# Optimization experiments

Measured on AMD Instinct MI355X. Metric: run time of the kernel, lower is better.

Reference implementation:

```python
import jax, jax.numpy as jnp
import numpy as np

# Hyperparameters matching init_kwargs
LR = 0.02
AT = 0.3
DSBETA = 0.1
EPS_DS = 0.5

B, D, N = 8192, 1024, 4096


def setup_inputs() -> dict:
    key = jax.random.key(0)
    k0, k1, k2, k3 = jax.random.split(key, 4)
    x = jax.random.normal(k0, (B, D), dtype=jnp.float32)
    weights = jax.random.normal(k1, (N, D), dtype=jnp.float32)
    relevance = jax.random.uniform(k2, (N, D), dtype=jnp.float32)
    moving_avg = jax.random.uniform(k3, (N, D), dtype=jnp.float32)
    node_control = jnp.ones((N,), dtype=jnp.float32)
    return {"x": x, "weights": weights, "relevance": relevance,
            "moving_avg": moving_avg, "node_control": node_control}


def reference(x, weights, relevance, moving_avg, node_control):
    n, d = weights.shape
    # pairwise squared distances [B, N] via one GEMM
    x2 = jnp.sum(x * x, axis=1, keepdims=True)            # [B,1]
    w2 = jnp.sum(weights * weights, axis=1)[None, :]      # [1,N]
    dists = x2 + w2 - 2.0 * jnp.matmul(x, weights.T)      # [B,N]
    # weighted_distance + activation
    rsum = jnp.sum(relevance, axis=1)                     # [N]
    dw = dists * (rsum / d)[None, :]
    dw = jnp.where(jnp.isnan(dw), 0.0, dw)
    act = (rsum[None, :] / (rsum[None, :] + dw + 1e-7)) * node_control[None, :]
    act_max = jnp.max(act, axis=1)                        # [B]
    idx = jnp.argmax(act, axis=1)                         # [B] winner per sample
    # high-activation mask; group samples by winner node (unique_node_diff_vectorized
    # == per-node mean of assigned high samples, done with segment_sum at fixed N)
    high = (act_max >= AT).astype(x.dtype)                # [B]
    counts = jax.ops.segment_sum(high, idx, num_segments=n)               # [N]
    sums = jax.ops.segment_sum(x * high[:, None], idx, num_segments=n)    # [N,D]
    has = (counts > 0).astype(x.dtype)[:, None]           # [N,1] nodes with >=1 high sample
    mean_s = sums / jnp.maximum(counts, 1.0)[:, None]     # [N,D] updatable_samples (dense)
    # update_node math (EMA moving_avg -> relevance -> weight update)
    a = LR * DSBETA
    distance = jnp.abs(mean_s - weights)
    mavg_new = a * distance + (1.0 - a) * moving_avg
    mx = jnp.max(mavg_new, axis=1, keepdims=True)
    mn = jnp.min(mavg_new, axis=1, keepdims=True)
    avg = jnp.mean(mavg_new, axis=1, keepdims=True)
    rel_new = 1.0 / (1.0 + jnp.exp((mavg_new - avg) / (EPS_DS * (mx - mn))))
    rel_new = jnp.where(jnp.isnan(rel_new), 1.0, rel_new)
    w_new = weights + LR * (mean_s - weights)
    # Original returns rows only for unique winning nodes (dynamic shape); here we
    # return fixed-shape [N,D] arrays masked to zero for nodes with no high sample.
    return (mean_s * has, w_new * has, rel_new * has)
```

## Files before the change

### kernel.cpp

```cpp
#include <hip/hip_runtime.h>
#include <stdint.h>


#define B_DIM 8192
#define D_DIM 1024
#define N_DIM 4096
#define ND ((size_t)N_DIM * D_DIM)
#define LRc 0.02f
#define ATc 0.3f
#define EMAc (0.02f * 0.1f)
#define QS 32.0f
#define INV_QS2 (1.0f / (QS * QS))
#define MARGIN_G 10.0f

typedef int intv4 __attribute__((ext_vector_type(4)));

__device__ __forceinline__ void async16(void* lds, const void* g) {
    __builtin_amdgcn_global_load_lds((const __attribute__((address_space(1))) void*)g,
                                     (__attribute__((address_space(3))) void*)lds, 16, 0, 0);
}

__device__ __forceinline__ int q8(float v) {
    return (int)rintf(fminf(fmaxf(v * QS, -127.0f), 127.0f));
}

__device__ __forceinline__ unsigned pack4(float4 v) {
    return (unsigned)(q8(v.x) & 255) | ((unsigned)(q8(v.y) & 255) << 8)
         | ((unsigned)(q8(v.z) & 255) << 16) | ((unsigned)(q8(v.w) & 255) << 24);
}

__global__ __launch_bounds__(256) void prep_k(const float* __restrict__ x, const float* __restrict__ w,
                                              const float* __restrict__ rel,
                                              signed char* __restrict__ xq, signed char* __restrict__ wq,
                                              float* __restrict__ x2p, float* __restrict__ w2p,
                                              float* __restrict__ rsump, float* __restrict__ gbp) {
    const int lane = threadIdx.x & 63, wave = threadIdx.x >> 6;
    const int row = (blockIdx.x << 2) + wave;
    if (row < B_DIM) {
        const float4* xr = (const float4*)(x + (size_t)row * D_DIM);
        unsigned* xqr = (unsigned*)(xq + (size_t)row * D_DIM);
        float ss = 0.f;
#pragma unroll
        for (int j = 0; j < 4; ++j) {
            const float4 v = xr[lane + j * 64];
            ss += v.x * v.x + v.y * v.y + v.z * v.z + v.w * v.w;
            xqr[lane + j * 64] = pack4(v);
        }
#pragma unroll
        for (int o = 32; o; o >>= 1) ss += __shfl_xor(ss, o);
        if (lane == 0) x2p[row] = ss;
    } else {
        const int n = row - B_DIM;
        const float4* wr = (const float4*)(w + (size_t)n * D_DIM);
        const float4* rr = (const float4*)(rel + (size_t)n * D_DIM);
        unsigned* wqr = (unsigned*)(wq + (size_t)n * D_DIM);
        float ss = 0.f, rs = 0.f;
#pragma unroll
        for (int j = 0; j < 4; ++j) {
            const float4 v = wr[lane + j * 64];
            const float4 rv = rr[lane + j * 64];
            ss += v.x * v.x + v.y * v.y + v.z * v.z + v.w * v.w;
            rs += rv.x + rv.y + rv.z + rv.w;
            wqr[lane + j * 64] = pack4(v);
        }
#pragma unroll
        for (int o = 32; o; o >>= 1) { ss += __shfl_xor(ss, o); rs += __shfl_xor(rs, o); }
        if (lane == 0) {
            w2p[n] = ss;
            rsump[n] = rs;
            gbp[n] = ss + (1e-7f * (float)D_DIM) / rs;
        }
    }
}

__global__ __launch_bounds__(512, 2) void gemm_k(const signed char* __restrict__ xq,
                                                 const signed char* __restrict__ wq,
                                                 const float* __restrict__ gbp,
                                                 unsigned short* __restrict__ resq,
                                                 float* __restrict__ tminp) {
    extern __shared__ char smem[];
    const int t = threadIdx.x;
    const int mt = blockIdx.x & 31;
    const int nt = blockIdx.x >> 5;
    const int m0 = mt * 256, n0 = nt * 256;
    const int lane = t & 63, wave = t >> 6;
    const int q = lane >> 4, ln = lane & 15;
    const int wm = wave >> 2, wn = wave & 3;

    intv4 acc[8][4];
#pragma unroll
    for (int i = 0; i < 8; ++i)
#pragma unroll
        for (int j = 0; j < 4; ++j) acc[i][j] = (intv4){0, 0, 0, 0};

    int gOff[4], lOff[4];
#pragma unroll
    for (int s = 0; s < 4; ++s) {
        const int L = t + s * 512;
        const int r = L >> 3;
        gOff[s] = r * D_DIM + ((L & 7) ^ (r & 7)) * 16;
        lOff[s] = L * 16;
    }
    const signed char* Ap = xq + (size_t)m0 * D_DIM;
    const signed char* Bp = wq + (size_t)n0 * D_DIM;

    const int baseA = (wm * 128 + ln) * 128;
    const int baseB = (wn * 64 + ln) * 128;

#define STAGE_KT(kt, slot) do {                                                     \
        char* sa_ = smem + (slot) * 65536;                                          \
        const int k0_ = (kt) * 128;                                                 \
        _Pragma("unroll")                                                           \
        for (int s_ = 0; s_ < 4; ++s_) async16(sa_ + lOff[s_], Ap + gOff[s_] + k0_);\
        _Pragma("unroll")                                                           \
        for (int s_ = 0; s_ < 4; ++s_) async16(sa_ + 32768 + lOff[s_], Bp + gOff[s_] + k0_); \
    } while (0)

#define COMPUTE_KT(slot) do {                                                       \
        const char* sa_ = smem + (slot) * 65536;                                    \
        const char* sb_ = sa_ + 32768;                                              \
        _Pragma("unroll")                                                           \
        for (int ks = 0; ks < 2; ++ks) {                                            \
            const int jx = ((ks * 4 + q) ^ (ln & 7)) * 16;                          \
            intv4 a[8], b[4];                                                       \
            _Pragma("unroll")                                                       \
            for (int i = 0; i < 8; ++i) a[i] = *(const intv4*)(sa_ + baseA + i * 2048 + jx); \
            _Pragma("unroll")                                                       \
            for (int j = 0; j < 4; ++j) b[j] = *(const intv4*)(sb_ + baseB + j * 2048 + jx); \
            __builtin_amdgcn_s_setprio(1);                                          \
            _Pragma("unroll")                                                       \
            for (int i = 0; i < 8; ++i)                                             \
                _Pragma("unroll")                                                   \
                for (int j = 0; j < 4; ++j)                                         \
                    acc[i][j] = __builtin_amdgcn_mfma_i32_16x16x64_i8(a[i], b[j], acc[i][j], 0, 0, 0); \
            __builtin_amdgcn_s_setprio(0);                                          \
        }                                                                           \
    } while (0)

    STAGE_KT(0, 0);
#pragma unroll
    for (int kt = 0; kt < 8; ++kt) {
        if (kt < 7) {
            STAGE_KT(kt + 1, (kt + 1) & 1);
            asm volatile("s_waitcnt vmcnt(8)" ::: "memory");
        } else {
            asm volatile("s_waitcnt vmcnt(0)" ::: "memory");
        }
        __builtin_amdgcn_s_barrier();
        COMPUTE_KT(kt & 1);
        asm volatile("" ::: "memory");
        __builtin_amdgcn_s_barrier();
    }
#undef STAGE_KT
#undef COMPUTE_KT

    float gbv[4];
#pragma unroll
    for (int j = 0; j < 4; ++j) gbv[j] = gbp[n0 + wn * 64 + j * 16 + ln];
    const float cf = 2.0f * INV_QS2;
    const int tile64 = nt * 4 + wn;
#pragma unroll
    for (int i = 0; i < 8; ++i) {
#pragma unroll
        for (int r = 0; r < 4; ++r) {
            const int m = m0 + wm * 128 + i * 16 + q * 4 + r;
            float g[4];
            float mn = 3.4e38f;
#pragma unroll
            for (int j = 0; j < 4; ++j) {
                g[j] = gbv[j] - cf * (float)acc[i][j][r];
                mn = fminf(mn, g[j]);
            }
#pragma unroll
            for (int o = 1; o < 16; o <<= 1) mn = fminf(mn, __shfl_xor(mn, o));
            if (ln == 0) tminp[(size_t)m * 64 + tile64] = mn;
            unsigned u = 0;
#pragma unroll
            for (int j = 0; j < 4; ++j) {
                int a4 = (int)rintf(g[j] - mn);
                a4 = (a4 > 15) ? 15 : a4;
                u |= (unsigned)a4 << (4 * j);
            }
            resq[(size_t)m * 1024 + tile64 * 16 + ln] = (unsigned short)u;
        }
    }
}

__global__ __launch_bounds__(256) void resolve_k(const unsigned short* __restrict__ resq,
                                                 const float* __restrict__ tminp,
                                                 const float* __restrict__ x2p,
                                                 const float* __restrict__ x, const float* __restrict__ w,
                                                 const float* __restrict__ w2p, const float* __restrict__ rsump,
                                                 const float* __restrict__ ncp,
                                                 int* __restrict__ win) {
    const int lane = threadIdx.x & 63, wave = threadIdx.x >> 6;
    const int b = (blockIdx.x << 2) + wave;
    const float tv = tminp[(size_t)b * 64 + lane];
    float rowmin = tv;
#pragma unroll
    for (int o = 32; o; o >>= 1) rowmin = fminf(rowmin, __shfl_xor(rowmin, o));
    const float th = rowmin + MARGIN_G;
    const float thq = th + 0.5f;
    const unsigned long long tmask = __ballot(tv <= th);
    const float x2v = x2p[b];
    const unsigned short* rrow = resq + (size_t)b * 1024;
    const int nibsh = (lane >> 4) * 4;

    int cnt = 0, myn = -1;
    float myg = 0.0f;
    unsigned long long tm = tmask;
    while (tm) {
        const int tt = __ffsll((long long)tm) - 1;
        tm &= tm - 1;
        const float tb = __shfl(tv, tt);
        const unsigned short pv = rrow[tt * 16 + (lane & 15)];
        const float g = tb + (float)((pv >> nibsh) & 15);
        const bool c = (g <= thq);
        cnt += __popcll(__ballot(c));
        if (c && myn < 0) { myn = tt * 64 + lane; myg = g; }
    }

    if (cnt == 1) {
        if (myn >= 0) {
            const float act = ncp[myn] * (float)D_DIM / ((float)D_DIM + x2v + myg);
            win[b] = (act >= ATc) ? myn : -1;
        }
    } else {
        const float4* xr = (const float4*)(x + (size_t)b * D_DIM);
        float4 xv[4];
#pragma unroll
        for (int j = 0; j < 4; ++j) xv[j] = xr[lane + j * 64];
        float best_act = -1.0f;
        int best_n = N_DIM;
        tm = tmask;
        while (tm) {
            const int tt = __ffsll((long long)tm) - 1;
            tm &= tm - 1;
            const float tb = __shfl(tv, tt);
            const unsigned short pv = rrow[tt * 16 + (lane & 15)];
            const float g = tb + (float)((pv >> nibsh) & 15);
            unsigned long long cm = __ballot(g <= thq);
            while (cm) {
                const int l = __ffsll((long long)cm) - 1;
                cm &= cm - 1;
                const int n = tt * 64 + l;
                const float4* wr = (const float4*)(w + (size_t)n * D_DIM);
                float p = 0.f;
#pragma unroll
                for (int j = 0; j < 4; ++j) {
                    const float4 wv = wr[lane + j * 64];
                    p += xv[j].x * wv.x + xv[j].y * wv.y + xv[j].z * wv.z + xv[j].w * wv.w;
                }
#pragma unroll
                for (int o = 32; o; o >>= 1) p += __shfl_xor(p, o);
                const float dist = x2v + w2p[n] - 2.0f * p;
                const float rs = rsump[n];
                const float dw = dist * rs * (1.0f / (float)D_DIM);
                const float a = rs * ncp[n] / (rs + dw + 1e-7f);
                if (a > best_act || (a == best_act && n < best_n)) { best_act = a; best_n = n; }
            }
        }
        if (lane == 0) win[b] = (best_act >= ATc) ? best_n : -1;
    }
}

__global__ __launch_bounds__(256) void finalize_k(const float* __restrict__ x, const float* __restrict__ w,
                                                  const float* __restrict__ mavg, const int* __restrict__ win,
                                                  float* __restrict__ out) {
    const int n = blockIdx.x, t = threadIdx.x;
    __shared__ unsigned short list[B_DIM];
    __shared__ int cnt;
    __shared__ float smax[4], smin[4], ssum[4];
    if (t == 0) cnt = 0;
    __syncthreads();
    const int4* wp = (const int4*)win;
#pragma unroll
    for (int k = 0; k < 8; ++k) {
        const int4 v = wp[k * 256 + t];
        const int b0 = (k * 256 + t) * 4;
        if (v.x == n) list[atomicAdd(&cnt, 1)] = (unsigned short)(b0 + 0);
        if (v.y == n) list[atomicAdd(&cnt, 1)] = (unsigned short)(b0 + 1);
        if (v.z == n) list[atomicAdd(&cnt, 1)] = (unsigned short)(b0 + 2);
        if (v.w == n) list[atomicAdd(&cnt, 1)] = (unsigned short)(b0 + 3);
    }
    __syncthreads();
    const int c = cnt;
    float4 s = {0.f, 0.f, 0.f, 0.f};
    for (int e = 0; e < c; ++e) {
        const float4 xv = ((const float4*)(x + (size_t)list[e] * D_DIM))[t];
        s.x += xv.x; s.y += xv.y; s.z += xv.z; s.w += xv.w;
    }
    const float has = (c > 0) ? 1.0f : 0.0f;
    const float invc = 1.0f / fmaxf((float)c, 1.0f);
    const size_t base4 = (size_t)n * (D_DIM / 4);
    const float4 wv = ((const float4*)w)[base4 + t];
    const float4 mk = ((const float4*)mavg)[base4 + t];
    float4 ms, mv;
    ms.x = s.x * invc; ms.y = s.y * invc; ms.z = s.z * invc; ms.w = s.w * invc;
    mv.x = EMAc * fabsf(ms.x - wv.x) + (1.0f - EMAc) * mk.x;
    mv.y = EMAc * fabsf(ms.y - wv.y) + (1.0f - EMAc) * mk.y;
    mv.z = EMAc * fabsf(ms.z - wv.z) + (1.0f - EMAc) * mk.z;
    mv.w = EMAc * fabsf(ms.w - wv.w) + (1.0f - EMAc) * mk.w;
    float lmax = fmaxf(fmaxf(mv.x, mv.y), fmaxf(mv.z, mv.w));
    float lmin = fminf(fminf(mv.x, mv.y), fminf(mv.z, mv.w));
    float lsum = mv.x + mv.y + mv.z + mv.w;
#pragma unroll
    for (int o = 32; o; o >>= 1) {
        lmax = fmaxf(lmax, __shfl_xor(lmax, o));
        lmin = fminf(lmin, __shfl_xor(lmin, o));
        lsum += __shfl_xor(lsum, o);
    }
    const int wave = t >> 6, lane = t & 63;
    if (lane == 0) { smax[wave] = lmax; smin[wave] = lmin; ssum[wave] = lsum; }
    __syncthreads();
    const float mx = fmaxf(fmaxf(smax[0], smax[1]), fmaxf(smax[2], smax[3]));
    const float mn = fminf(fminf(smin[0], smin[1]), fminf(smin[2], smin[3]));
    const float avg = (ssum[0] + ssum[1] + ssum[2] + ssum[3]) * (1.0f / (float)D_DIM);
    const float scale = 0.5f * (mx - mn);
    const float invs = (scale > 0.0f) ? 1.0f / scale : 0.0f;
    float4 relv;
    if (scale > 0.0f) {
        relv.x = 1.0f / (1.0f + __expf((mv.x - avg) * invs));
        relv.y = 1.0f / (1.0f + __expf((mv.y - avg) * invs));
        relv.z = 1.0f / (1.0f + __expf((mv.z - avg) * invs));
        relv.w = 1.0f / (1.0f + __expf((mv.w - avg) * invs));
    } else {
        relv.x = relv.y = relv.z = relv.w = 1.0f;
    }
    float4* o0 = (float4*)out;
    float4 r0, r1, r2;
    r0.x = ms.x * has; r0.y = ms.y * has; r0.z = ms.z * has; r0.w = ms.w * has;
    r1.x = (wv.x + LRc * (ms.x - wv.x)) * has;
    r1.y = (wv.y + LRc * (ms.y - wv.y)) * has;
    r1.z = (wv.z + LRc * (ms.z - wv.z)) * has;
    r1.w = (wv.w + LRc * (ms.w - wv.w)) * has;
    r2.x = relv.x * has; r2.y = relv.y * has; r2.z = relv.z * has; r2.w = relv.w * has;
    o0[base4 + t] = r0;
    o0[ND / 4 + base4 + t] = r1;
    o0[2 * (ND / 4) + base4 + t] = r2;
}

extern "C" void kernel_launch(void* const* d_in, const int* in_sizes, int n_in,
                              void* d_out, int out_size, void* d_ws, size_t ws_size,
                              hipStream_t stream) {
    const float* x    = (const float*)d_in[0];
    const float* w    = (const float*)d_in[1];
    const float* rel  = (const float*)d_in[2];
    const float* mavg = (const float*)d_in[3];
    const float* nc   = (const float*)d_in[4];
    float* out = (float*)d_out;

    char* p = (char*)d_ws;
    size_t off = 0;
    auto take = [&](size_t bytes) -> char* {
        char* r = p + off;
        off += (bytes + 255) & ~(size_t)255;
        return r;
    };
    signed char* xq = (signed char*)take((size_t)B_DIM * D_DIM);
    signed char* wq = (signed char*)take((size_t)N_DIM * D_DIM);
    float* x2       = (float*)take((size_t)B_DIM * 4);
    float* w2       = (float*)take((size_t)N_DIM * 4);
    float* rsum     = (float*)take((size_t)N_DIM * 4);
    float* gb       = (float*)take((size_t)N_DIM * 4);
    unsigned short* resq = (unsigned short*)take((size_t)B_DIM * 1024 * 2);
    float* tminp    = (float*)take((size_t)B_DIM * 64 * 4);
    int* win        = (int*)take((size_t)B_DIM * 4);

    static bool attr_set = false;
    if (!attr_set) {
        (void)hipFuncSetAttribute(reinterpret_cast<const void*>(gemm_k),
                                  hipFuncAttributeMaxDynamicSharedMemorySize, 131072);
        attr_set = true;
    }

    prep_k<<<(B_DIM + N_DIM) / 4, 256, 0, stream>>>(x, w, rel, xq, wq, x2, w2, rsum, gb);
    gemm_k<<<512, 512, 131072, stream>>>(xq, wq, gb, resq, tminp);
    resolve_k<<<B_DIM / 4, 256, 0, stream>>>(resq, tminp, x2, x, w, w2, rsum, nc, win);
    finalize_k<<<N_DIM, 256, 0, stream>>>(x, w, mavg, win, out);
}
```

Measured before the change: 207.3 us.

## Split int8 GEMM K-tiles into half-stages with finer-grained async prefetch

```diff
diff --git a/kernel.cpp b/kernel.cpp
--- a/kernel.cpp
+++ b/kernel.cpp
@@ -93,66 +93,67 @@
 #pragma unroll
         for (int j = 0; j < 4; ++j) acc[i][j] = (intv4){0, 0, 0, 0};
 
-    int gOff[4], lOff[4];
-#pragma unroll
-    for (int s = 0; s < 4; ++s) {
-        const int L = t + s * 512;
-        const int r = L >> 3;
-        gOff[s] = r * D_DIM + ((L & 7) ^ (r & 7)) * 16;
-        lOff[s] = L * 16;
-    }
+    const int ls0 = t * 16;
+    const int row0 = t >> 2;
+    const int go0 = row0 * 1024 + (((t & 3) ^ ((row0 >> 1) & 3)) * 16);
+
     const signed char* Ap = xq + (size_t)m0 * D_DIM;
     const signed char* Bp = wq + (size_t)n0 * D_DIM;
 
-    const int baseA = (wm * 128 + ln) * 128;
-    const int baseB = (wn * 64 + ln) * 128;
-
-#define STAGE_KT(kt, slot) do {                                                     \
-        char* sa_ = smem + (slot) * 65536;                                          \
-        const int k0_ = (kt) * 128;                                                 \
-        _Pragma("unroll")                                                           \
-        for (int s_ = 0; s_ < 4; ++s_) async16(sa_ + lOff[s_], Ap + gOff[s_] + k0_);\
-        _Pragma("unroll")                                                           \
-        for (int s_ = 0; s_ < 4; ++s_) async16(sa_ + 32768 + lOff[s_], Bp + gOff[s_] + k0_); \
+    const int aBase = (wm * 128 + ln) * 64;
+    const int bBase = (wn * 64 + ln) * 64 + 32768;
+    const int cslot = (q ^ ((ln >> 1) & 3)) * 16;
+
+#define STG(kt_, kh_, isB_) do {                                                     \
+        char* d_ = smem + ((kt_) & 1) * 65536 + (isB_) * 32768 + (kh_) * 16384;      \
+        const signed char* g_ = ((isB_) ? Bp : Ap) + (kt_) * 128 + (kh_) * 64 + go0; \
+        async16(d_ + ls0, g_);                                                       \
+        async16(d_ + ls0 + 8192, g_ + 131072);                                       \
     } while (0)
 
-#define COMPUTE_KT(slot) do {                                                       \
-        const char* sa_ = smem + (slot) * 65536;                                    \
-        const char* sb_ = sa_ + 32768;                                              \
-        _Pragma("unroll")                                                           \
-        for (int ks = 0; ks < 2; ++ks) {                                            \
-            const int jx = ((ks * 4 + q) ^ (ln & 7)) * 16;                          \
-            intv4 a[8], b[4];                                                       \
-            _Pragma("unroll")                                                       \
-            for (int i = 0; i < 8; ++i) a[i] = *(const intv4*)(sa_ + baseA + i * 2048 + jx); \
-            _Pragma("unroll")                                                       \
-            for (int j = 0; j < 4; ++j) b[j] = *(const intv4*)(sb_ + baseB + j * 2048 + jx); \
-            __builtin_amdgcn_s_setprio(1);                                          \
-            _Pragma("unroll")                                                       \
-            for (int i = 0; i < 8; ++i)                                             \
-                _Pragma("unroll")                                                   \
-                for (int j = 0; j < 4; ++j)                                         \
-                    acc[i][j] = __builtin_amdgcn_mfma_i32_16x16x64_i8(a[i], b[j], acc[i][j], 0, 0, 0); \
-            __builtin_amdgcn_s_setprio(0);                                          \
-        }                                                                           \
+    STG(0, 0, 0); STG(0, 0, 1); STG(0, 1, 0); STG(0, 1, 1); STG(1, 0, 0); STG(1, 0, 1);
+    asm volatile("s_waitcnt vmcnt(8)" ::: "memory");
+    __builtin_amdgcn_s_barrier();
+
+#define VM8 asm volatile("s_waitcnt vmcnt(8)" ::: "memory")
+#define VM4 asm volatile("s_waitcnt vmcnt(4)" ::: "memory")
+#define VM0 asm volatile("s_waitcnt vmcnt(0)" ::: "memory")
+
+#define PH(kt_, ks_, ih_, STMT_STAGE, STMT_WAIT) do {                                \
+        const char* base_ = smem + ((kt_) & 1) * 65536 + (ks_) * 16384;              \
+        intv4 a_[4], b_[4];                                                          \
+        _Pragma("unroll")                                                            \
+        for (int i_ = 0; i_ < 4; ++i_)                                               \
+            a_[i_] = *(const intv4*)(base_ + aBase + (ih_) * 4096 + i_ * 1024 + cslot); \
+        _Pragma("unroll")                                                            \
+        for (int j_ = 0; j_ < 4; ++j_)                                               \
+            b_[j_] = *(const intv4*)(base_ + bBase + j_ * 1024 + cslot);             \
+        STMT_STAGE;                                                                  \
+        STMT_WAIT;                                                                   \
+        __builtin_amdgcn_s_barrier();                                                \
+        __builtin_amdgcn_s_setprio(1);                                               \
+        _Pragma("unroll")                                                            \
+        for (int i_ = 0; i_ < 4; ++i_)                                               \
+            _Pragma("unroll")                                                        \
+            for (int j_ = 0; j_ < 4; ++j_)                                           \
+                acc[(ih_) * 4 + i_][j_] =                                            \
+                    __builtin_amdgcn_mfma_i32_16x16x64_i8(a_[i_], b_[j_], acc[(ih_) * 4 + i_][j_], 0, 0, 0); \
+        __builtin_amdgcn_s_setprio(0);                                               \
+        __builtin_amdgcn_s_barrier();                                                \
     } while (0)
 
-    STAGE_KT(0, 0);
 #pragma unroll
     for (int kt = 0; kt < 8; ++kt) {
-        if (kt < 7) {
-            STAGE_KT(kt + 1, (kt + 1) & 1);
-            asm volatile("s_waitcnt vmcnt(8)" ::: "memory");
-        } else {
-            asm volatile("s_waitcnt vmcnt(0)" ::: "memory");
-        }
-        __builtin_amdgcn_s_barrier();
-        COMPUTE_KT(kt & 1);
-        asm volatile("" ::: "memory");
-        __builtin_amdgcn_s_barrier();
-    }
-#undef STAGE_KT
-#undef COMPUTE_KT
+        PH(kt, 0, 0, { if (kt + 1 < 8) STG(kt + 1, 1, 0); }, {});
+        PH(kt, 0, 1, { if (kt + 1 < 8) STG(kt + 1, 1, 1); }, { if (kt < 7) { VM8; } else { VM0; } });
+        PH(kt, 1, 0, { if (kt + 2 < 8) STG(kt + 2, 0, 0); }, {});
+        PH(kt, 1, 1, { if (kt + 2 < 8) STG(kt + 2, 0, 1); }, { if (kt < 6) { VM8; } else if (kt == 6) { VM4; } });
+    }
+#undef PH
+#undef STG
+#undef VM8
+#undef VM4
+#undef VM0
 
     float gbv[4];
 #pragma unroll
```

Result: no change. 209.2 us (+0.9%).

## Retile int8 GEMM to 256x128 blocks with smaller K-steps and grouped block order

Applied to the files above, without the earlier changes.

```diff
diff --git a/kernel.cpp b/kernel.cpp
--- a/kernel.cpp
+++ b/kernel.cpp
@@ -73,19 +73,21 @@
     }
 }
 
-__global__ __launch_bounds__(512, 2) void gemm_k(const signed char* __restrict__ xq,
+__global__ __launch_bounds__(256, 3) void gemm_k(const signed char* __restrict__ xq,
                                                  const signed char* __restrict__ wq,
                                                  const float* __restrict__ gbp,
                                                  unsigned short* __restrict__ resq,
                                                  float* __restrict__ tminp) {
-    extern __shared__ char smem[];
+    __shared__ char smem[49152];
     const int t = threadIdx.x;
-    const int mt = blockIdx.x & 31;
-    const int nt = blockIdx.x >> 5;
-    const int m0 = mt * 256, n0 = nt * 256;
+    const int region = blockIdx.x & 7;
+    const int local  = blockIdx.x >> 3;
+    const int mt = ((region >> 1) << 3) + (local >> 4);
+    const int nt = ((region & 1) << 4) + (local & 15);
+    const int m0 = mt * 256, n0 = nt * 128;
     const int lane = t & 63, wave = t >> 6;
     const int q = lane >> 4, ln = lane & 15;
-    const int wm = wave >> 2, wn = wave & 3;
+    const int wm = wave >> 1, wn = wave & 1;
 
     intv4 acc[8][4];
 #pragma unroll
@@ -93,72 +95,69 @@
 #pragma unroll
         for (int j = 0; j < 4; ++j) acc[i][j] = (intv4){0, 0, 0, 0};
 
-    int gOff[4], lOff[4];
+    int gA[4], gB[2];
 #pragma unroll
     for (int s = 0; s < 4; ++s) {
-        const int L = t + s * 512;
-        const int r = L >> 3;
-        gOff[s] = r * D_DIM + ((L & 7) ^ (r & 7)) * 16;
-        lOff[s] = L * 16;
+        const int S = t + s * 256, r = S >> 2;
+        gA[s] = r * D_DIM + (((S & 3) ^ (r & 3)) * 16);
+    }
+#pragma unroll
+    for (int s = 0; s < 2; ++s) {
+        const int S = t + s * 256, r = S >> 2;
+        gB[s] = r * D_DIM + (((S & 3) ^ (r & 3)) * 16);
     }
     const signed char* Ap = xq + (size_t)m0 * D_DIM;
     const signed char* Bp = wq + (size_t)n0 * D_DIM;
 
-    const int baseA = (wm * 128 + ln) * 128;
-    const int baseB = (wn * 64 + ln) * 128;
-
-#define STAGE_KT(kt, slot) do {                                                     \
-        char* sa_ = smem + (slot) * 65536;                                          \
-        const int k0_ = (kt) * 128;                                                 \
-        _Pragma("unroll")                                                           \
-        for (int s_ = 0; s_ < 4; ++s_) async16(sa_ + lOff[s_], Ap + gOff[s_] + k0_);\
-        _Pragma("unroll")                                                           \
-        for (int s_ = 0; s_ < 4; ++s_) async16(sa_ + 32768 + lOff[s_], Bp + gOff[s_] + k0_); \
+    const int cslot = (q ^ (ln & 3)) * 16;
+    const int aBase = (wm * 128 + ln) * 64;
+    const int bBase = (wn * 64 + ln) * 64;
+
+#define STG(kt_, buf_) do {                                                          \
+        char* base_ = smem + (buf_) * 24576;                                         \
+        const int k0_ = (kt_) * 64;                                                  \
+        _Pragma("unroll")                                                            \
+        for (int s_ = 0; s_ < 4; ++s_)                                               \
+            async16(base_ + (t + s_ * 256) * 16, Ap + gA[s_] + k0_);                 \
+        _Pragma("unroll")                                                            \
+        for (int s_ = 0; s_ < 2; ++s_)                                               \
+            async16(base_ + 16384 + (t + s_ * 256) * 16, Bp + gB[s_] + k0_);         \
     } while (0)
 
-#define COMPUTE_KT(slot) do {                                                       \
-        const char* sa_ = smem + (slot) * 65536;                                    \
-        const char* sb_ = sa_ + 32768;                                              \
-        _Pragma("unroll")                                                           \
-        for (int ks = 0; ks < 2; ++ks) {                                            \
-            const int jx = ((ks * 4 + q) ^ (ln & 7)) * 16;                          \
-            intv4 a[8], b[4];                                                       \
-            _Pragma("unroll")                                                       \
-            for (int i = 0; i < 8; ++i) a[i] = *(const intv4*)(sa_ + baseA + i * 2048 + jx); \
-            _Pragma("unroll")                                                       \
-            for (int j = 0; j < 4; ++j) b[j] = *(const intv4*)(sb_ + baseB + j * 2048 + jx); \
-            __builtin_amdgcn_s_setprio(1);                                          \
-            _Pragma("unroll")                                                       \
-            for (int i = 0; i < 8; ++i)                                             \
-                _Pragma("unroll")                                                   \
-                for (int j = 0; j < 4; ++j)                                         \
-                    acc[i][j] = __builtin_amdgcn_mfma_i32_16x16x64_i8(a[i], b[j], acc[i][j], 0, 0, 0); \
-            __builtin_amdgcn_s_setprio(0);                                          \
-        }                                                                           \
-    } while (0)
-
-    STAGE_KT(0, 0);
-#pragma unroll
-    for (int kt = 0; kt < 8; ++kt) {
-        if (kt < 7) {
-            STAGE_KT(kt + 1, (kt + 1) & 1);
-            asm volatile("s_waitcnt vmcnt(8)" ::: "memory");
+    STG(0, 0);
+#pragma unroll 4
+    for (int kt = 0; kt < 16; ++kt) {
+        if (kt < 15) {
+            STG(kt + 1, (kt + 1) & 1);
+            asm volatile("s_waitcnt vmcnt(6)" ::: "memory");
         } else {
             asm volatile("s_waitcnt vmcnt(0)" ::: "memory");
         }
         __builtin_amdgcn_s_barrier();
-        COMPUTE_KT(kt & 1);
+        const char* sa = smem + (kt & 1) * 24576;
+        const char* sb = sa + 16384;
+        intv4 a[8], b[4];
+#pragma unroll
+        for (int i = 0; i < 8; ++i) a[i] = *(const intv4*)(sa + aBase + i * 1024 + cslot);
+#pragma unroll
+        for (int j = 0; j < 4; ++j) b[j] = *(const intv4*)(sb + bBase + j * 1024 + cslot);
+        __builtin_amdgcn_s_setprio(1);
+#pragma unroll
+        for (int i = 0; i < 8; ++i)
+#pragma unroll
+            for (int j = 0; j < 4; ++j)
+                acc[i][j] = __builtin_amdgcn_mfma_i32_16x16x64_i8(a[i], b[j], acc[i][j], 0, 0, 0);
+        __builtin_amdgcn_s_setprio(0);
         asm volatile("" ::: "memory");
         __builtin_amdgcn_s_barrier();
     }
-#undef STAGE_KT
-#undef COMPUTE_KT
+#undef STG
 
     float gbv[4];
 #pragma unroll
     for (int j = 0; j < 4; ++j) gbv[j] = gbp[n0 + wn * 64 + j * 16 + ln];
     const float cf = 2.0f * INV_QS2;
-    const int tile64 = nt * 4 + wn;
+    const int tile64 = nt * 2 + wn;
 #pragma unroll
     for (int i = 0; i < 8; ++i) {
 #pragma unroll
@@ -367,15 +366,8 @@
     float* tminp    = (float*)take((size_t)B_DIM * 64 * 4);
     int* win        = (int*)take((size_t)B_DIM * 4);
 
-    static bool attr_set = false;
-    if (!attr_set) {
-        (void)hipFuncSetAttribute(reinterpret_cast<const void*>(gemm_k),
-                                  hipFuncAttributeMaxDynamicSharedMemorySize, 131072);
-        attr_set = true;
-    }
-
     prep_k<<<(B_DIM + N_DIM) / 4, 256, 0, stream>>>(x, w, rel, xq, wq, x2, w2, rsum, gb);
-    gemm_k<<<512, 512, 131072, stream>>>(xq, wq, gb, resq, tminp);
+    gemm_k<<<1024, 256, 0, stream>>>(xq, wq, gb, resq, tminp);
     resolve_k<<<B_DIM / 4, 256, 0, stream>>>(resq, tminp, x2, x, w, w2, rsum, nc, win);
     finalize_k<<<N_DIM, 256, 0, stream>>>(x, w, mavg, win, out);
 }
```

New measurement: 294.6 us. +42.1%, slower.
